# Kernel optimization log

Measured on AMD Instinct MI355X. Metric: run time of the kernel, lower is better.

Reference implementation:

```python
import jax, jax.numpy as jnp
import numpy as np

B, S, D = 4, 2048, 2048
H, HD = 16, 128
ROPE_THETA = 10000.0


def rotate_half(x):
    half = x.shape[-1] // 2
    return jnp.concatenate([-x[..., half:], x[..., :half]], axis=-1)


def setup_inputs() -> dict:
    key = jax.random.key(0)
    ks = jax.random.split(key, 5)
    scale = 1.0 / np.sqrt(D)
    x = jax.random.normal(ks[0], (B, S, D), dtype=jnp.float32)
    wq = jax.random.normal(ks[1], (D, H * HD), dtype=jnp.float32) * scale
    wk = jax.random.normal(ks[2], (D, H * HD), dtype=jnp.float32) * scale
    wv = jax.random.normal(ks[3], (D, H * HD), dtype=jnp.float32) * scale
    wo = jax.random.normal(ks[4], (H * HD, D), dtype=jnp.float32) * scale
    # RoPE frequencies: freqs_cis real/imag parts, shape [S, HD//2]
    inv_freq = 1.0 / (ROPE_THETA ** (np.arange(0, HD, 2, dtype=np.float32) / HD))
    t = np.arange(S, dtype=np.float32)
    freqs = np.outer(t, inv_freq)  # [S, HD//2]
    cos = jnp.asarray(np.cos(freqs), dtype=jnp.float32)
    sin = jnp.asarray(np.sin(freqs), dtype=jnp.float32)
    return {"x": x, "wq": wq, "wk": wk, "wv": wv, "wo": wo, "cos": cos, "sin": sin}


def reference(x, wq, wk, wv, wo, cos, sin):
    batch, seq_len, _ = x.shape
    # QKV projections (no bias), reshape to [b, h, s, d]
    q = (x @ wq).reshape(batch, seq_len, H, HD).transpose(0, 2, 1, 3)
    k = (x @ wk).reshape(batch, seq_len, H, HD).transpose(0, 2, 1, 3)
    v = (x @ wv).reshape(batch, seq_len, H, HD)  # [b, s, h, d]
    # RoPE (half-split / rotate_half convention)
    cos_full = jnp.concatenate([cos, cos], axis=-1)[None, None, :seq_len, :]
    sin_full = jnp.concatenate([sin, sin], axis=-1)[None, None, :seq_len, :]
    q = q * cos_full + rotate_half(q) * sin_full
    k = k * cos_full + rotate_half(k) * sin_full
    # Scaled dot-product attention with causal mask
    logits = jnp.einsum('bhqd,bhkd->bhqk', q, k) / jnp.sqrt(jnp.float32(HD))
    causal = jnp.tril(jnp.ones((seq_len, seq_len), dtype=bool))
    logits = jnp.where(causal[None, None, :, :], logits, -1e10)
    weights = jax.nn.softmax(logits, axis=-1)
    out = jnp.einsum('bhqk,bkhd->bqhd', weights, v)
    out = out.reshape(batch, seq_len, H * HD)
    return out @ wo
```

## Files before the change

### kernel.cpp

```cpp
#include <hip/hip_runtime.h>
#include <cstdint>
#include <cstddef>

typedef unsigned short u16;
using bf16x8  = __attribute__((ext_vector_type(8))) short;
using floatx4 = __attribute__((ext_vector_type(4))) float;

__device__ __forceinline__ u16 f2bf(float f) {
    union { float f; unsigned u; } v; v.f = f;
    unsigned r = v.u + 0x7fffu + ((v.u >> 16) & 1u);
    return (u16)(r >> 16);
}
__device__ __forceinline__ float bf2f(u16 h) {
    union { unsigned u; float f; } v; v.u = ((unsigned)h) << 16; return v.f;
}
__device__ __forceinline__ floatx4 mfma16(bf16x8 a, bf16x8 b, floatx4 c) {
    return __builtin_amdgcn_mfma_f32_16x16x32_bf16(a, b, c, 0, 0, 0);
}
using gptr_t = const __attribute__((address_space(1))) unsigned int*;
using lptr_t = __attribute__((address_space(3))) unsigned int*;
__device__ __forceinline__ void lds16(const void* g, void* l) {
    __builtin_amdgcn_global_load_lds((gptr_t)g, (lptr_t)l, 16, 0, 0);
}
typedef __attribute__((address_space(3))) const u16* lds_cp;
__device__ __forceinline__ bf16x8 dsr128(const u16* p) {
    bf16x8 r;
    asm volatile("ds_read_b128 %0, %1" : "=v"(r) : "v"((lds_cp)p));
    return r;
}

#define ATT_SCALE 0.1275758218522532f

__global__ __launch_bounds__(256) void cvt_x(const float* __restrict__ x, u16* __restrict__ xb) {
    size_t i = ((size_t)blockIdx.x * 256 + threadIdx.x) * 4;
    float4 v = *(const float4*)&x[i];
    ushort4 r; r.x = f2bf(v.x); r.y = f2bf(v.y); r.z = f2bf(v.z); r.w = f2bf(v.w);
    *(ushort4*)&xb[i] = r;
}

__global__ __launch_bounds__(256) void transpose_wall(const float* __restrict__ wq, const float* __restrict__ wk,
                                                      const float* __restrict__ wv, const float* __restrict__ wo,
                                                      u16* __restrict__ wqkvb, u16* __restrict__ wob) {
    __shared__ float t[64][65];
    const int z = blockIdx.z;
    const float* in = (z == 0) ? wq : (z == 1) ? wk : (z == 2) ? wv : wo;
    u16* out = (z < 3) ? (wqkvb + (size_t)z * 2048 * 2048) : wob;
    int k0 = blockIdx.x * 64, n0 = blockIdx.y * 64;
    int tx = threadIdx.x, ty = threadIdx.y;
#pragma unroll
    for (int i = 0; i < 16; ++i) {
        int r = i * 4 + ty;
        t[r][tx] = in[(size_t)(k0 + r) * 2048 + n0 + tx];
    }
    __syncthreads();
#pragma unroll
    for (int i = 0; i < 16; ++i) {
        int r = i * 4 + ty;
        out[(size_t)(n0 + r) * 2048 + k0 + tx] = f2bf(t[tx][r]);
    }
}

template <int MODE>
__global__ __launch_bounds__(512, 2) void gemm_bt(const u16* __restrict__ A, const u16* __restrict__ B,
                                                  u16* __restrict__ Qo, u16* __restrict__ Ko, u16* __restrict__ Vt,
                                                  float* __restrict__ Co,
                                                  const float* __restrict__ cosb, const float* __restrict__ sinb) {
    __shared__ __align__(16) u16 sA[2][16384];
    __shared__ __align__(16) u16 sB[2][16384];

    const int nbx = (MODE == 0) ? 24 : 8;
    const int bid = blockIdx.x;
    const int q8 = (int)gridDim.x >> 3;
    const int wg = (bid & 7) * q8 + (bid >> 3);
    const int bx = wg % nbx, by = wg / nbx;
    const int m0 = by << 8, n0 = bx << 8;

    const int tid = threadIdx.x;
    const int w = tid >> 6, lane = tid & 63;
    const int wm = w >> 2, wn = w & 3;
    const int m16 = lane & 15, q4 = lane >> 4;
    const int lr = lane >> 3;
    const int lc8 = (lane & 7) ^ lr;
    const int wnbase = (wn >> 1) * 128 + (wn & 1) * 32;

    const u16* Ag = A + (size_t)(m0 + w * 16 + lr) * 2048 + lc8 * 8;
    const u16* Bg = B + (size_t)(n0 + w * 16 + lr) * 2048 + lc8 * 8;

    const int swz0 = ((q4 ^ (m16 & 7)) << 3);
    const int swz1 = (((4 + q4) ^ (m16 & 7)) << 3);

    floatx4 acc[8][4];
#pragma unroll
    for (int r = 0; r < 8; ++r)
#pragma unroll
        for (int c = 0; c < 4; ++c) acc[r][c] = (floatx4)0.0f;
    bf16x8 af[4][2];
    bf16x8 bf[4][2];

#define STAGE_A(b, h, t) do { \
    lds16(Ag + (size_t)((h) * 128) * 2048 + (t) * 64,     &sA[b][(h) * 8192 + w * 1024]);       \
    lds16(Ag + (size_t)((h) * 128 + 8) * 2048 + (t) * 64, &sA[b][(h) * 8192 + w * 1024 + 512]); \
} while (0)
#define STAGE_B(b, h, t) do { \
    lds16(Bg + (size_t)((h) * 128) * 2048 + (t) * 64,     &sB[b][(h) * 8192 + w * 1024]);       \
    lds16(Bg + (size_t)((h) * 128 + 8) * 2048 + (t) * 64, &sB[b][(h) * 8192 + w * 1024 + 512]); \
} while (0)
#define BAR() __builtin_amdgcn_s_barrier()
#define WAITL0() do { asm volatile("s_waitcnt lgkmcnt(0)" ::: "memory"); __builtin_amdgcn_sched_barrier(0); } while (0)
#define WAITL8() asm volatile("s_waitcnt lgkmcnt(8)" ::: "memory")
#define LDA_(cur, mq) do { _Pragma("unroll") for (int fr = 0; fr < 4; ++fr) { \
    const u16* p = &sA[cur][(wm * 128 + (mq) * 64 + fr * 16 + m16) * 64];      \
    af[fr][0] = dsr128(&p[swz0]);                                              \
    af[fr][1] = dsr128(&p[swz1]); } } while (0)
#define LDB_(cur, nq) do { _Pragma("unroll") for (int c = 0; c < 2; ++c) {     \
    const int j = (nq) * 2 + c;                                                \
    const u16* p = &sB[cur][(wnbase + (j & 1) * 16 + (j >> 1) * 64 + m16) * 64]; \
    bf[j][0] = dsr128(&p[swz0]);                                               \
    bf[j][1] = dsr128(&p[swz1]); } } while (0)
#define MM_(mq, nq) do { _Pragma("unroll") for (int kk = 0; kk < 2; ++kk)      \
    _Pragma("unroll") for (int fr = 0; fr < 4; ++fr)                           \
    _Pragma("unroll") for (int c = 0; c < 2; ++c)                              \
        acc[(mq) * 4 + fr][(nq) * 2 + c] =                                     \
            mfma16(af[fr][kk], bf[(nq) * 2 + c][kk], acc[(mq) * 4 + fr][(nq) * 2 + c]); } while (0)

    const int NT = 32;

    STAGE_B(0, 0, 0); STAGE_B(0, 1, 0);
    STAGE_A(0, 0, 0); STAGE_A(0, 1, 0);
    STAGE_B(1, 0, 1); STAGE_B(1, 1, 1);
    asm volatile("s_waitcnt vmcnt(4)" ::: "memory");
    __builtin_amdgcn_s_barrier();

#pragma unroll 2
    for (int t = 0; t < NT; ++t) {
        const int cur = t & 1;
        LDB_(cur, 0);
        LDA_(cur, 0);
        if (t + 1 < NT) STAGE_A(cur ^ 1, 0, t + 1);
        WAITL8();
        BAR();
        WAITL0();
        __builtin_amdgcn_s_setprio(1); MM_(0, 0); __builtin_amdgcn_s_setprio(0);
        BAR();
        LDB_(cur, 1);
        if (t + 1 < NT) STAGE_A(cur ^ 1, 1, t + 1);
        BAR();
        WAITL0();
        __builtin_amdgcn_s_setprio(1); MM_(0, 1); __builtin_amdgcn_s_setprio(0);
        BAR();
        LDA_(cur, 1);
        if (t + 2 < NT) STAGE_B(cur, 0, t + 2);
        BAR();
        WAITL0();
        __builtin_amdgcn_s_setprio(1); MM_(1, 1); __builtin_amdgcn_s_setprio(0);
        BAR();
        if (t + 2 < NT) STAGE_B(cur, 1, t + 2);
        BAR();
        __builtin_amdgcn_s_setprio(1); MM_(1, 0); __builtin_amdgcn_s_setprio(0);
        if (t + 2 < NT)      { asm volatile("s_waitcnt vmcnt(4)" ::: "memory"); }
        else if (t + 1 < NT) { asm volatile("s_waitcnt vmcnt(0)" ::: "memory"); }
        BAR();
    }

#undef STAGE_A
#undef STAGE_B
#undef BAR
#undef WAITL0
#undef WAITL8
#undef LDA_
#undef LDB_
#undef MM_

    if (MODE == 0) {
        const int which = n0 >> 11;
        if (which < 2) {
            u16* dst = (which == 0) ? Qo : Ko;
            const float sc = (which == 0) ? ATT_SCALE : 1.0f;
            const int h = ((n0 >> 7) + (wn >> 1)) & 15;
            const int dp0 = (wn & 1) * 32 + m16;
#pragma unroll
            for (int fr = 0; fr < 8; ++fr) {
                const int mb = m0 + wm * 128 + fr * 16 + q4 * 4;
#pragma unroll
                for (int c0 = 0; c0 < 2; ++c0) {
                    const int dp = dp0 + c0 * 16;
#pragma unroll
                    for (int i = 0; i < 4; ++i) {
                        const int mm = mb + i;
                        const int b = mm >> 11, s = mm & 2047;
                        const float cs = cosb[(size_t)s * 64 + dp];
                        const float sn = sinb[(size_t)s * 64 + dp];
                        const float lo = acc[fr][c0][i], hi = acc[fr][c0 + 2][i];
                        const size_t base = ((size_t)((b * 16 + h) * 2048 + s) << 7) + dp;
                        dst[base]      = f2bf((lo * cs - hi * sn) * sc);
                        dst[base + 64] = f2bf((hi * cs + lo * sn) * sc);
                    }
                }
            }
        } else {
#pragma unroll
            for (int fr = 0; fr < 8; ++fr) {
                const int mb = m0 + wm * 128 + fr * 16 + q4 * 4;
                const int b = mb >> 11, s = mb & 2047;
#pragma unroll
                for (int c = 0; c < 4; ++c) {
                    const int n = n0 + wnbase + (c & 1) * 16 + (c >> 1) * 64 + m16;
                    const int h = (n >> 7) & 15, d = n & 127;
                    ushort4 pk;
                    pk.x = f2bf(acc[fr][c][0]); pk.y = f2bf(acc[fr][c][1]);
                    pk.z = f2bf(acc[fr][c][2]); pk.w = f2bf(acc[fr][c][3]);
                    *(ushort4*)&Vt[((size_t)((b * 16 + h) * 128 + d)) * 2048 + s] = pk;
                }
            }
        }
    } else {
#pragma unroll
        for (int fr = 0; fr < 8; ++fr) {
            const int mb = m0 + wm * 128 + fr * 16 + q4 * 4;
#pragma unroll
            for (int c = 0; c < 4; ++c) {
                const int n = n0 + wnbase + (c & 1) * 16 + (c >> 1) * 64 + m16;
#pragma unroll
                for (int i = 0; i < 4; ++i)
                    Co[(size_t)(mb + i) * 2048 + n] = acc[fr][c][i];
            }
        }
    }
}

__global__ __launch_bounds__(512) void attn_kernel(const u16* __restrict__ Q, const u16* __restrict__ K,
                                                   const u16* __restrict__ VT, u16* __restrict__ AO) {
    __shared__ __align__(16) u16 ks[64 * 136];
    __shared__ __align__(16) u16 vts[128 * 72];
    __shared__ __align__(16) u16 ps[256 * 72];
    static const int iqmap[8] = {7, 6, 5, 4, 0, 1, 2, 3};
    const int bx = blockIdx.x;
    const int iq = iqmap[bx >> 6];
    const int bh = bx & 63;
    const int b = bh >> 4, h = bh & 15;
    const u16* Qg = Q  + (size_t)bh * (2048 * 128);
    const u16* Kg = K  + (size_t)bh * (2048 * 128);
    const u16* Vg = VT + (size_t)bh * (128 * 2048);
    const int tid = threadIdx.x, w = tid >> 6, lane = tid & 63;
    const int m16 = lane & 15, q4 = lane >> 4;
    const int jn = 4 * iq + 4;

    const int qrow = iq * 256 + w * 32;
    bf16x8 qf[2][4];
#pragma unroll
    for (int rm = 0; rm < 2; ++rm)
#pragma unroll
        for (int kk = 0; kk < 4; ++kk)
            qf[rm][kk] = *(const bf16x8*)&Qg[(size_t)(qrow + rm * 16 + m16) * 128 + kk * 32 + q4 * 8];

    floatx4 o[2][8];
#pragma unroll
    for (int rm = 0; rm < 2; ++rm)
#pragma unroll
        for (int c = 0; c < 8; ++c) o[rm][c] = (floatx4)0.0f;
    float mrow[2] = {-1e30f, -1e30f}, lrow[2] = {0.0f, 0.0f};

    const int kr0 = tid >> 4,          kc0 = tid & 15;
    const int kr1 = (512 + tid) >> 4,  kc1 = tid & 15;
    const int vr0 = tid >> 3,          vc0 = tid & 7;
    const int vr1 = (512 + tid) >> 3,  vc1 = tid & 7;
    uint4 kreg0, kreg1, vreg0, vreg1;

#define LOADKV(j) do { \
    kreg0 = *(const uint4*)&Kg[(size_t)((j) * 64 + kr0) * 128 + kc0 * 8]; \
    kreg1 = *(const uint4*)&Kg[(size_t)((j) * 64 + kr1) * 128 + kc1 * 8]; \
    vreg0 = *(const uint4*)&Vg[(size_t)vr0 * 2048 + (j) * 64 + vc0 * 8];  \
    vreg1 = *(const uint4*)&Vg[(size_t)vr1 * 2048 + (j) * 64 + vc1 * 8];  \
} while (0)

    LOADKV(0);

    for (int j = 0; j < jn; ++j) {
        asm volatile("" ::: "memory");
        __builtin_amdgcn_s_barrier();
        asm volatile("" ::: "memory");
        *(uint4*)&ks[kr0 * 136 + kc0 * 8] = kreg0;
        *(uint4*)&ks[kr1 * 136 + kc1 * 8] = kreg1;
        *(uint4*)&vts[vr0 * 72 + vc0 * 8] = vreg0;
        *(uint4*)&vts[vr1 * 72 + vc1 * 8] = vreg1;
        if (j + 1 < jn) LOADKV(j + 1);
        asm volatile("s_waitcnt lgkmcnt(0)" ::: "memory");
        __builtin_amdgcn_s_barrier();
        asm volatile("" ::: "memory");

        floatx4 sacc[2][4];
#pragma unroll
        for (int rm = 0; rm < 2; ++rm)
#pragma unroll
            for (int r = 0; r < 4; ++r) sacc[rm][r] = (floatx4)0.0f;
        __builtin_amdgcn_s_setprio(1);
#pragma unroll
        for (int kk = 0; kk < 4; ++kk) {
            bf16x8 kb[4];
#pragma unroll
            for (int r = 0; r < 4; ++r)
                kb[r] = *(const bf16x8*)&ks[(r * 16 + m16) * 136 + kk * 32 + q4 * 8];
#pragma unroll
            for (int rm = 0; rm < 2; ++rm)
#pragma unroll
                for (int r = 0; r < 4; ++r)
                    sacc[rm][r] = mfma16(kb[r], qf[rm][kk], sacc[rm][r]);
        }
        __builtin_amdgcn_s_setprio(0);

        if (j >= 4 * iq) {
#pragma unroll
            for (int rm = 0; rm < 2; ++rm) {
                const int qg = qrow + rm * 16 + m16;
#pragma unroll
                for (int r = 0; r < 4; ++r)
#pragma unroll
                    for (int i = 0; i < 4; ++i) {
                        int kg = j * 64 + r * 16 + q4 * 4 + i;
                        if (kg > qg) sacc[rm][r][i] = -1e30f;
                    }
            }
        }

#pragma unroll
        for (int rm = 0; rm < 2; ++rm) {
            float pmax = -1e30f;
#pragma unroll
            for (int r = 0; r < 4; ++r)
#pragma unroll
                for (int i = 0; i < 4; ++i) pmax = fmaxf(pmax, sacc[rm][r][i]);
            pmax = fmaxf(pmax, __shfl_xor(pmax, 16));
            pmax = fmaxf(pmax, __shfl_xor(pmax, 32));
            float mnew = fmaxf(mrow[rm], pmax);
            float alpha = __builtin_amdgcn_exp2f(mrow[rm] - mnew);
            mrow[rm] = mnew;

            float psum = 0.0f;
#pragma unroll
            for (int r = 0; r < 4; ++r) {
                float p0 = __builtin_amdgcn_exp2f(sacc[rm][r][0] - mnew);
                float p1 = __builtin_amdgcn_exp2f(sacc[rm][r][1] - mnew);
                float p2 = __builtin_amdgcn_exp2f(sacc[rm][r][2] - mnew);
                float p3 = __builtin_amdgcn_exp2f(sacc[rm][r][3] - mnew);
                psum += (p0 + p1) + (p2 + p3);
                ushort4 pk; pk.x = f2bf(p0); pk.y = f2bf(p1); pk.z = f2bf(p2); pk.w = f2bf(p3);
                *(ushort4*)&ps[(w * 32 + rm * 16 + m16) * 72 + r * 16 + q4 * 4] = pk;
            }
            psum += __shfl_xor(psum, 16);
            psum += __shfl_xor(psum, 32);
            lrow[rm] = lrow[rm] * alpha + psum;

            float abc[4];
#pragma unroll
            for (int i = 0; i < 4; ++i) abc[i] = __shfl(alpha, q4 * 4 + i);
#pragma unroll
            for (int c = 0; c < 8; ++c)
#pragma unroll
                for (int i = 0; i < 4; ++i) o[rm][c][i] *= abc[i];
        }

#pragma unroll
        for (int kk = 0; kk < 2; ++kk) {
            bf16x8 pa[2];
#pragma unroll
            for (int rm = 0; rm < 2; ++rm)
                pa[rm] = *(const bf16x8*)&ps[(w * 32 + rm * 16 + m16) * 72 + kk * 32 + q4 * 8];
            __builtin_amdgcn_s_setprio(1);
#pragma unroll
            for (int ch = 0; ch < 2; ++ch) {
                bf16x8 vb[4];
#pragma unroll
                for (int c = 0; c < 4; ++c)
                    vb[c] = *(const bf16x8*)&vts[((ch * 4 + c) * 16 + m16) * 72 + kk * 32 + q4 * 8];
#pragma unroll
                for (int rm = 0; rm < 2; ++rm)
#pragma unroll
                    for (int c = 0; c < 4; ++c)
                        o[rm][ch * 4 + c] = mfma16(pa[rm], vb[c], o[rm][ch * 4 + c]);
            }
            __builtin_amdgcn_s_setprio(0);
        }
    }
#undef LOADKV

#pragma unroll
    for (int rm = 0; rm < 2; ++rm) {
        float linv = __builtin_amdgcn_rcpf(lrow[rm]);
        float li[4];
#pragma unroll
        for (int i = 0; i < 4; ++i) li[i] = __shfl(linv, q4 * 4 + i);
#pragma unroll
        for (int c = 0; c < 8; ++c)
#pragma unroll
            for (int i = 0; i < 4; ++i) {
                int s = qrow + rm * 16 + q4 * 4 + i;
                int d = c * 16 + m16;
                AO[((size_t)(b * 2048 + s)) * 2048 + h * 128 + d] = f2bf(o[rm][c][i] * li[i]);
            }
    }
}

extern "C" void kernel_launch(void* const* d_in, const int* in_sizes, int n_in,
                              void* d_out, int out_size, void* d_ws, size_t ws_size,
                              hipStream_t stream) {
    const float* x    = (const float*)d_in[0];
    const float* wq   = (const float*)d_in[1];
    const float* wk   = (const float*)d_in[2];
    const float* wv   = (const float*)d_in[3];
    const float* wo   = (const float*)d_in[4];
    const float* cosb = (const float*)d_in[5];
    const float* sinb = (const float*)d_in[6];
    float* out = (float*)d_out;

    char* ws = (char*)d_ws;
    u16* xb    = (u16*)(ws);
    u16* AO    = xb;
    u16* wqkvb = (u16*)(ws + 33554432);
    u16* wob   = (u16*)(ws + 58720256);
    u16* Qb    = (u16*)(ws + 67108864);
    u16* Kb    = (u16*)(ws + 100663296);
    u16* Vtb   = (u16*)(ws + 134217728);

    cvt_x<<<16384, 256, 0, stream>>>(x, xb);
    transpose_wall<<<dim3(32, 32, 4), dim3(64, 4), 0, stream>>>(wq, wk, wv, wo, wqkvb, wob);

    gemm_bt<0><<<768, 512, 0, stream>>>(xb, wqkvb, Qb, Kb, Vtb, nullptr, cosb, sinb);
    attn_kernel<<<512, 512, 0, stream>>>(Qb, Kb, Vtb, AO);
    gemm_bt<1><<<256, 512, 0, stream>>>(AO, wob, nullptr, nullptr, nullptr, out, nullptr, nullptr);
}
```

Before: 548.2 us.

## Load K and V MFMA fragments directly from global memory, dropping LDS staging

The attention kernel stops staging K and V tiles through shared memory with register prefetch and block barriers. Each wave now reads its K and V MFMA operands straight from global memory, relying on L1/L2 caching, and the V fragments for a tile are loaded before the softmax. Launch bounds now request two blocks per CU. Removing the K/V LDS buffers and barriers cuts synchronisation and LDS use, but all eight waves re-read the same K/V tile from global memory, adding cache traffic and latency that is no longer software-pipelined.

```diff
diff --git a/kernel.cpp b/kernel.cpp
--- a/kernel.cpp
+++ b/kernel.cpp
@@ -228,10 +228,8 @@
     }
 }
 
-__global__ __launch_bounds__(512) void attn_kernel(const u16* __restrict__ Q, const u16* __restrict__ K,
-                                                   const u16* __restrict__ VT, u16* __restrict__ AO) {
-    __shared__ __align__(16) u16 ks[64 * 136];
-    __shared__ __align__(16) u16 vts[128 * 72];
+__global__ __launch_bounds__(512, 2) void attn_kernel(const u16* __restrict__ Q, const u16* __restrict__ K,
+                                                      const u16* __restrict__ VT, u16* __restrict__ AO) {
     __shared__ __align__(16) u16 ps[256 * 72];
     static const int iqmap[8] = {7, 6, 5, 4, 0, 1, 2, 3};
     const int bx = blockIdx.x;
@@ -260,53 +258,33 @@
         for (int c = 0; c < 8; ++c) o[rm][c] = (floatx4)0.0f;
     float mrow[2] = {-1e30f, -1e30f}, lrow[2] = {0.0f, 0.0f};
 
-    const int kr0 = tid >> 4,          kc0 = tid & 15;
-    const int kr1 = (512 + tid) >> 4,  kc1 = tid & 15;
-    const int vr0 = tid >> 3,          vc0 = tid & 7;
-    const int vr1 = (512 + tid) >> 3,  vc1 = tid & 7;
-    uint4 kreg0, kreg1, vreg0, vreg1;
-
-#define LOADKV(j) do { \
-    kreg0 = *(const uint4*)&Kg[(size_t)((j) * 64 + kr0) * 128 + kc0 * 8]; \
-    kreg1 = *(const uint4*)&Kg[(size_t)((j) * 64 + kr1) * 128 + kc1 * 8]; \
-    vreg0 = *(const uint4*)&Vg[(size_t)vr0 * 2048 + (j) * 64 + vc0 * 8];  \
-    vreg1 = *(const uint4*)&Vg[(size_t)vr1 * 2048 + (j) * 64 + vc1 * 8];  \
-} while (0)
-
-    LOADKV(0);
-
     for (int j = 0; j < jn; ++j) {
-        asm volatile("" ::: "memory");
-        __builtin_amdgcn_s_barrier();
-        asm volatile("" ::: "memory");
-        *(uint4*)&ks[kr0 * 136 + kc0 * 8] = kreg0;
-        *(uint4*)&ks[kr1 * 136 + kc1 * 8] = kreg1;
-        *(uint4*)&vts[vr0 * 72 + vc0 * 8] = vreg0;
-        *(uint4*)&vts[vr1 * 72 + vc1 * 8] = vreg1;
-        if (j + 1 < jn) LOADKV(j + 1);
-        asm volatile("s_waitcnt lgkmcnt(0)" ::: "memory");
-        __builtin_amdgcn_s_barrier();
-        asm volatile("" ::: "memory");
-
         floatx4 sacc[2][4];
 #pragma unroll
         for (int rm = 0; rm < 2; ++rm)
 #pragma unroll
             for (int r = 0; r < 4; ++r) sacc[rm][r] = (floatx4)0.0f;
-        __builtin_amdgcn_s_setprio(1);
 #pragma unroll
         for (int kk = 0; kk < 4; ++kk) {
             bf16x8 kb[4];
 #pragma unroll
             for (int r = 0; r < 4; ++r)
-                kb[r] = *(const bf16x8*)&ks[(r * 16 + m16) * 136 + kk * 32 + q4 * 8];
+                kb[r] = *(const bf16x8*)&Kg[(size_t)(j * 64 + r * 16 + m16) * 128 + kk * 32 + q4 * 8];
+            __builtin_amdgcn_s_setprio(1);
 #pragma unroll
             for (int rm = 0; rm < 2; ++rm)
 #pragma unroll
                 for (int r = 0; r < 4; ++r)
                     sacc[rm][r] = mfma16(kb[r], qf[rm][kk], sacc[rm][r]);
-        }
-        __builtin_amdgcn_s_setprio(0);
+            __builtin_amdgcn_s_setprio(0);
+        }
+
+        bf16x8 vb[2][8];
+#pragma unroll
+        for (int kk = 0; kk < 2; ++kk)
+#pragma unroll
+            for (int c8 = 0; c8 < 8; ++c8)
+                vb[kk][c8] = *(const bf16x8*)&Vg[(size_t)(c8 * 16 + m16) * 2048 + j * 64 + kk * 32 + q4 * 8];
 
         if (j >= 4 * iq) {
 #pragma unroll
@@ -367,21 +345,13 @@
                 pa[rm] = *(const bf16x8*)&ps[(w * 32 + rm * 16 + m16) * 72 + kk * 32 + q4 * 8];
             __builtin_amdgcn_s_setprio(1);
 #pragma unroll
-            for (int ch = 0; ch < 2; ++ch) {
-                bf16x8 vb[4];
-#pragma unroll
-                for (int c = 0; c < 4; ++c)
-                    vb[c] = *(const bf16x8*)&vts[((ch * 4 + c) * 16 + m16) * 72 + kk * 32 + q4 * 8];
+            for (int c8 = 0; c8 < 8; ++c8)
 #pragma unroll
                 for (int rm = 0; rm < 2; ++rm)
-#pragma unroll
-                    for (int c = 0; c < 4; ++c)
-                        o[rm][ch * 4 + c] = mfma16(pa[rm], vb[c], o[rm][ch * 4 + c]);
-            }
+                    o[rm][c8] = mfma16(pa[rm], vb[kk][c8], o[rm][c8]);
             __builtin_amdgcn_s_setprio(0);
         }
     }
-#undef LOADKV
 
 #pragma unroll
     for (int rm = 0; rm < 2; ++rm) {
```

New measurement: 735.8 us. 34.2% more time.
